# Kernel tuning notes

Measured on AMD Instinct MI355X. Metric: run time of the kernel, lower is better.

The kernel has to match this reference:

```python
import jax, jax.numpy as jnp
import numpy as np

VOCAB = 100000
E = 300          # embedding_size
S = 128          # seq_len
B = 8192         # batch
H1 = 2048
H2 = 2048
C = 1221         # num_classes
PAD = 1          # padding token id (sentence trimmed after last non-1 token)


def setup_inputs() -> dict:
    key = jax.random.key(0)
    ks = jax.random.split(key, 8)
    x = jax.random.randint(ks[0], (S, B), 0, VOCAB, dtype=jnp.int64 if jax.config.jax_enable_x64 else jnp.int32)
    emb = jax.random.normal(ks[1], (VOCAB, E), dtype=jnp.float32) * 0.1
    W1 = jax.random.normal(ks[2], (H1, 2 * E), dtype=jnp.float32) * (1.0 / np.sqrt(2 * E))
    b1 = jnp.zeros((H1,), dtype=jnp.float32)
    W2 = jax.random.normal(ks[3], (H2, H1), dtype=jnp.float32) * (1.0 / np.sqrt(H1))
    b2 = jnp.zeros((H2,), dtype=jnp.float32)
    W_out = jax.random.normal(ks[4], (C, H2), dtype=jnp.float32) * (1.0 / np.sqrt(H2))
    b_out = jnp.zeros((C,), dtype=jnp.float32)
    return {"x": x, "emb": emb, "W1": W1, "b1": b1, "W2": W2, "b2": b2,
            "W_out": W_out, "b_out": b_out}


def reference(x, emb, W1, b1, W2, b2, W_out, b_out):
    # x: [S, B] token ids -> transpose to [B, S] as in torch forward
    xb = x.T                                   # [B, S]
    nonpad = xb != PAD                         # [B, S]
    # index of LAST non-padding token per sentence (torch: (sent != 1).nonzero()[-1])
    last = (S - 1) - jnp.argmax(nonpad[:, ::-1], axis=1)      # [B]
    pos = jnp.arange(S)
    # sentence[:last+1] keeps everything up to and including `last`,
    # including any PAD tokens inside that prefix (faithful to the slice).
    mask = (pos[None, :] <= last[:, None]).astype(emb.dtype)  # [B, S]

    ex = emb[xb]                               # [B, S, E] embedding lookup
    mean = jnp.einsum('bse,bs->be', ex, mask) / jnp.sum(mask, axis=1, keepdims=True)
    feat = jnp.concatenate([ex[:, 0, :], mean], axis=1)       # [B, 2E] (FEE + avg)

    h = jax.nn.relu(feat @ W1.T + b1)          # [B, H1]
    h = jax.nn.relu(h @ W2.T + b2)             # [B, H2]
    out = h @ W_out.T + b_out                  # [B, C]
    return out
```

## Files before the change

kernel.cpp:

```cpp
#include <hip/hip_runtime.h>
#include <hip/hip_bf16.h>

#define S 128
#define BATCH 8192
#define E 300
#define KPAD 640
#define H1 2048
#define H2 2048
#define CLS 1221
#define CPAD 1280
#define PADTOK 1
#define VOCAB 100000

typedef __bf16 bf16x8 __attribute__((ext_vector_type(8)));
typedef float f32x16 __attribute__((ext_vector_type(16)));

__device__ __forceinline__ float b2f(ushort u) {
  union { unsigned int i; float f; } v; v.i = ((unsigned int)u) << 16; return v.f;
}
__device__ __forceinline__ ushort f2b(float f) {
  unsigned int i = __float_as_uint(f);
  unsigned int r = (i + 0x7FFFu + ((i >> 16) & 1u)) >> 16;
  return (ushort)r;
}
__device__ __forceinline__ void async16(const void* g, void* l) {
  __builtin_amdgcn_global_load_lds(
      (__attribute__((address_space(1))) void*)(void*)(const_cast<void*>(g)),
      (__attribute__((address_space(3))) void*)l, 16, 0, 0);
}

#define NQ_EMB (VOCAB * E / 4)
#define NQ_W1  (H1 * KPAD / 4)
#define NQ_W2  (H1 * H2 / 4)
#define NQ_WO  (CPAD * H2 / 4)
#define NQ_XT  (S * BATCH / 4)
#define NQ_TOT (NQ_EMB + NQ_W1 + NQ_W2 + NQ_WO + NQ_XT)

__global__ __launch_bounds__(256) void cvt_all(const float* __restrict__ Ein,
                                               ushort* __restrict__ Eb,
                                               const float* __restrict__ W1,
                                               ushort* __restrict__ W1p,
                                               const float* __restrict__ W2,
                                               ushort* __restrict__ W2b,
                                               const float* __restrict__ Wout,
                                               ushort* __restrict__ Woutp,
                                               const int* __restrict__ x,
                                               int* __restrict__ xT) {
  int q = blockIdx.x * 256 + threadIdx.x;
  if (q < NQ_EMB) {
    float4 v = ((const float4*)Ein)[q];
    ushort4 o;
    o.x = f2b(v.x); o.y = f2b(v.y); o.z = f2b(v.z); o.w = f2b(v.w);
    ((ushort4*)Eb)[q] = o;
    return;
  }
  q -= NQ_EMB;
  if (q < NQ_W1) {
    int row = q / 160;
    int k0 = (q - row * 160) * 4;
    ushort4 o; o.x = 0; o.y = 0; o.z = 0; o.w = 0;
    if (k0 < 2 * E) {
      float4 v = *(const float4*)(W1 + (size_t)row * (2 * E) + k0);
      o.x = f2b(v.x); o.y = f2b(v.y); o.z = f2b(v.z); o.w = f2b(v.w);
    }
    ((ushort4*)W1p)[q] = o;
    return;
  }
  q -= NQ_W1;
  if (q < NQ_W2) {
    float4 v = ((const float4*)W2)[q];
    ushort4 o;
    o.x = f2b(v.x); o.y = f2b(v.y); o.z = f2b(v.z); o.w = f2b(v.w);
    ((ushort4*)W2b)[q] = o;
    return;
  }
  q -= NQ_W2;
  if (q < NQ_WO) {
    int n = (q * 4) >> 11;
    ushort4 o; o.x = 0; o.y = 0; o.z = 0; o.w = 0;
    if (n < CLS) {
      float4 v = ((const float4*)Wout)[q];
      o.x = f2b(v.x); o.y = f2b(v.y); o.z = f2b(v.z); o.w = f2b(v.w);
    }
    ((ushort4*)Woutp)[q] = o;
    return;
  }
  q -= NQ_WO;
  if (q < NQ_XT) {
    int b = q >> 5;
    int t4 = (q & 31) * 4;
    int4 o;
    o.x = x[(size_t)(t4 + 0) * BATCH + b];
    o.y = x[(size_t)(t4 + 1) * BATCH + b];
    o.z = x[(size_t)(t4 + 2) * BATCH + b];
    o.w = x[(size_t)(t4 + 3) * BATCH + b];
    ((int4*)xT)[q] = o;
  }
}

__global__ __launch_bounds__(128) void embed_kernel(const int* __restrict__ xT,
                                                    const ushort* __restrict__ emb,
                                                    ushort* __restrict__ feat) {
  __shared__ uint offs[S];
  __shared__ unsigned long long masks[2];
  const int b = blockIdx.x;
  const int t = threadIdx.x;

  int tok = xT[b * S + t];
  offs[t] = (uint)tok * 600u;
  unsigned long long m = __ballot(tok != PADTOK);
  if ((t & 63) == 0) masks[t >> 6] = m;
  __syncthreads();

  unsigned long long m0 = masks[0], m1 = masks[1];
  int last;
  if (m1)      last = 127 - __clzll(m1);
  else if (m0) last = 63 - __clzll(m0);
  else         last = S - 1;
  const int n = last + 1;
  const float inv = 1.0f / (float)n;

  const int lane = t & 63;
  const int q0 = (t < 64) ? t : (11 + t);
  const bool has2 = (lane < 11);
  const int q1 = q0 + 64;
  const uint off0 = 4u * (uint)q0;
  const uint off1 = 4u * (uint)q1;
  const char* base = (const char*)emb;

  float a0 = 0.f, a1 = 0.f, a2 = 0.f, a3 = 0.f;
  int s = 0;
  for (; s + 16 <= n; s += 16) {
    uint o[16];
#pragma unroll
    for (int j = 0; j < 16; j++) o[j] = offs[s + j];
    ushort2 u[16];
#pragma unroll
    for (int j = 0; j < 16; j++) u[j] = *(const ushort2*)(base + (o[j] + off0));
    ushort2 v[16];
    if (has2) {
#pragma unroll
      for (int j = 0; j < 16; j++) v[j] = *(const ushort2*)(base + (o[j] + off1));
    }
#pragma unroll
    for (int j = 0; j < 16; j++) { a0 += b2f(u[j].x); a1 += b2f(u[j].y); }
    if (has2) {
#pragma unroll
      for (int j = 0; j < 16; j++) { a2 += b2f(v[j].x); a3 += b2f(v[j].y); }
    }
  }
  for (; s < n; s++) {
    uint o = offs[s];
    ushort2 u = *(const ushort2*)(base + (o + off0));
    a0 += b2f(u.x); a1 += b2f(u.y);
    if (has2) {
      ushort2 v0 = *(const ushort2*)(base + (o + off1));
      a2 += b2f(v0.x); a3 += b2f(v0.y);
    }
  }

  ushort* fr = feat + (size_t)b * KPAD;
  ushort2 mo; mo.x = f2b(a0 * inv); mo.y = f2b(a1 * inv);
  *(ushort2*)(fr + E + 2 * q0) = mo;
  if (has2) {
    ushort2 mo2; mo2.x = f2b(a2 * inv); mo2.y = f2b(a3 * inv);
    *(ushort2*)(fr + E + 2 * q1) = mo2;
  }
  const uint o0 = offs[0];
  *(ushort2*)(fr + 2 * q0) = *(const ushort2*)(base + (o0 + off0));
  if (has2) *(ushort2*)(fr + 2 * q1) = *(const ushort2*)(base + (o0 + off1));
  if (t < 20) {
    ushort2 z; z.x = 0; z.y = 0;
    *(ushort2*)(fr + 2 * E + 2 * t) = z;
  }
}

#define BM 128
#define BN 128
#define BK 64

template <bool RELU, bool NGUARD, bool FP32OUT>
__global__ __launch_bounds__(256) void gemm_bt(const ushort* __restrict__ A,
                                               const ushort* __restrict__ B,
                                               const float* __restrict__ bias,
                                               void* __restrict__ Cv,
                                               int K, int lda, int ldb, int ldc,
                                               int Nreal) {
  __shared__ __align__(16) ushort lA[BM * BK];
  __shared__ __align__(16) ushort lB[BN * BK];

  const int tid = threadIdx.x;
  const int wave = tid >> 6;
  const int lane = tid & 63;
  const int m0 = blockIdx.y * BM;
  const int n0 = blockIdx.x * BN;
  const int wm = (wave >> 1) * 64;
  const int wn = (wave & 1) * 64;

  f32x16 acc[2][2];
#pragma unroll
  for (int i = 0; i < 2; i++)
#pragma unroll
    for (int j = 0; j < 2; j++)
#pragma unroll
      for (int r = 0; r < 16; r++) acc[i][j][r] = 0.f;

  const int srow8 = lane >> 3;
  const int kcw = (lane & 7) ^ srow8;

  const int lr = lane & 31;
  const int lk = lane >> 5;
  const int lx = lr & 7;

  for (int k0 = 0; k0 < K; k0 += BK) {
#pragma unroll
    for (int j = 0; j < 4; j++) {
      const int g = wave * 4 + j;
      const int row = g * 8 + srow8;
      async16(A + (size_t)(m0 + row) * lda + k0 + kcw * 8, (void*)&lA[g * 512]);
      async16(B + (size_t)(n0 + row) * ldb + k0 + kcw * 8, (void*)&lB[g * 512]);
    }
    __syncthreads();

#pragma unroll
    for (int ks = 0; ks < 4; ks++) {
      const int kc = ks * 2 + lk;
      bf16x8 af[2], bfr[2];
#pragma unroll
      for (int mi = 0; mi < 2; mi++) {
        const int row = wm + mi * 32 + lr;
        af[mi] = *(const bf16x8*)&lA[(row * 8 + (kc ^ lx)) * 8];
      }
#pragma unroll
      for (int ni = 0; ni < 2; ni++) {
        const int row = wn + ni * 32 + lr;
        bfr[ni] = *(const bf16x8*)&lB[(row * 8 + (kc ^ lx)) * 8];
      }
#pragma unroll
      for (int mi = 0; mi < 2; mi++)
#pragma unroll
        for (int ni = 0; ni < 2; ni++)
          acc[mi][ni] = __builtin_amdgcn_mfma_f32_32x32x16_bf16(
              af[mi], bfr[ni], acc[mi][ni], 0, 0, 0);
    }
    __syncthreads();
  }

#pragma unroll
  for (int ni = 0; ni < 2; ni++) {
    const int col = n0 + wn + ni * 32 + lr;
    const bool ok = (!NGUARD) || (col < Nreal);
    const float bv = ok ? bias[col] : 0.f;
#pragma unroll
    for (int mi = 0; mi < 2; mi++) {
#pragma unroll
      for (int r = 0; r < 16; r++) {
        const int row = m0 + wm + mi * 32 + (r & 3) + 8 * (r >> 2) + 4 * lk;
        float v = acc[mi][ni][r] + bv;
        if (RELU) v = fmaxf(v, 0.f);
        if (ok) {
          if (FP32OUT) ((float*)Cv)[(size_t)row * ldc + col] = v;
          else         ((ushort*)Cv)[(size_t)row * ldc + col] = f2b(v);
        }
      }
    }
  }
}

extern "C" void kernel_launch(void* const* d_in, const int* in_sizes, int n_in,
                              void* d_out, int out_size, void* d_ws, size_t ws_size,
                              hipStream_t stream) {
  const int* x = (const int*)d_in[0];
  const float* emb = (const float*)d_in[1];
  const float* W1 = (const float*)d_in[2];
  const float* b1 = (const float*)d_in[3];
  const float* W2 = (const float*)d_in[4];
  const float* b2 = (const float*)d_in[5];
  const float* Wout = (const float*)d_in[6];
  const float* bout = (const float*)d_in[7];
  float* out = (float*)d_out;

  char* ws = (char*)d_ws;
  ushort* feat = (ushort*)ws;  ws += (size_t)BATCH * KPAD * 2;
  ushort* h1 = (ushort*)ws;    ws += (size_t)BATCH * H1 * 2;
  ushort* h2 = (ushort*)ws;    ws += (size_t)BATCH * H2 * 2;
  ushort* W1p = (ushort*)ws;   ws += (size_t)H1 * KPAD * 2;
  ushort* W2b = (ushort*)ws;   ws += (size_t)H2 * H1 * 2;
  ushort* Woutp = (ushort*)ws; ws += (size_t)CPAD * H2 * 2;
  ushort* Eb = (ushort*)ws;    ws += (size_t)VOCAB * E * 2;
  int* xT = (int*)ws;          ws += (size_t)S * BATCH * 4;

  cvt_all<<<(NQ_TOT + 255) / 256, 256, 0, stream>>>(emb, Eb, W1, W1p, W2, W2b,
                                                    Wout, Woutp, x, xT);
  embed_kernel<<<BATCH, S, 0, stream>>>(xT, Eb, feat);

  gemm_bt<true, false, false><<<dim3(H1 / BN, BATCH / BM), 256, 0, stream>>>(
      feat, W1p, b1, (void*)h1, KPAD, KPAD, KPAD, H1, H1);
  gemm_bt<true, false, false><<<dim3(H2 / BN, BATCH / BM), 256, 0, stream>>>(
      h1, W2b, b2, (void*)h2, H1, H1, H1, H2, H2);
  gemm_bt<false, true, true><<<dim3(CPAD / BN, BATCH / BM), 256, 0, stream>>>(
      h2, Woutp, bout, (void*)out, H2, H2, H2, CLS, CLS);
}
```

Measured before the change: 504.0 us.

## Split embedding sum across two waves by sequence parity with 8-byte loads

The embedding-mean kernel used to split the 300 columns across two waves, each reading 4-byte pairs. Now each wave covers the full row with 8-byte ushort4 loads and handles alternating sequence positions. The two partial sums are combined through shared memory after a barrier. This widens the loads and balances the sequence work, at the cost of one extra sync and an LDS reduction.

```diff
diff --git a/kernel.cpp b/kernel.cpp
--- a/kernel.cpp
+++ b/kernel.cpp
@@ -103,6 +103,7 @@
                                                     ushort* __restrict__ feat) {
   __shared__ uint offs[S];
   __shared__ unsigned long long masks[2];
+  __shared__ __align__(16) float part[76 * 4];
   const int b = blockIdx.x;
   const int t = threadIdx.x;
 
@@ -120,58 +121,84 @@
   const int n = last + 1;
   const float inv = 1.0f / (float)n;
 
+  const int w = t >> 6;
   const int lane = t & 63;
-  const int q0 = (t < 64) ? t : (11 + t);
-  const bool has2 = (lane < 11);
-  const int q1 = q0 + 64;
-  const uint off0 = 4u * (uint)q0;
-  const uint off1 = 4u * (uint)q1;
   const char* base = (const char*)emb;
+  const uint off0 = (uint)lane * 8u;
+  const bool tail = (lane < 11);
+  const uint off1 = 512u + (uint)lane * 8u;
 
   float a0 = 0.f, a1 = 0.f, a2 = 0.f, a3 = 0.f;
-  int s = 0;
-  for (; s + 16 <= n; s += 16) {
-    uint o[16];
-#pragma unroll
-    for (int j = 0; j < 16; j++) o[j] = offs[s + j];
-    ushort2 u[16];
-#pragma unroll
-    for (int j = 0; j < 16; j++) u[j] = *(const ushort2*)(base + (o[j] + off0));
-    ushort2 v[16];
-    if (has2) {
-#pragma unroll
-      for (int j = 0; j < 16; j++) v[j] = *(const ushort2*)(base + (o[j] + off1));
-    }
-#pragma unroll
-    for (int j = 0; j < 16; j++) { a0 += b2f(u[j].x); a1 += b2f(u[j].y); }
-    if (has2) {
-#pragma unroll
-      for (int j = 0; j < 16; j++) { a2 += b2f(v[j].x); a3 += b2f(v[j].y); }
-    }
-  }
-  for (; s < n; s++) {
+  float c0 = 0.f, c1 = 0.f, c2 = 0.f, c3 = 0.f;
+
+  int s = w;
+  for (; s + 14 < n; s += 16) {
+    uint o[8];
+#pragma unroll
+    for (int j = 0; j < 8; j++) o[j] = offs[s + 2 * j];
+    ushort4 u[8];
+#pragma unroll
+    for (int j = 0; j < 8; j++) u[j] = *(const ushort4*)(base + (o[j] + off0));
+    ushort4 v[8];
+    if (tail) {
+#pragma unroll
+      for (int j = 0; j < 8; j++) v[j] = *(const ushort4*)(base + (o[j] + off1));
+    }
+#pragma unroll
+    for (int j = 0; j < 8; j++) {
+      a0 += b2f(u[j].x); a1 += b2f(u[j].y);
+      a2 += b2f(u[j].z); a3 += b2f(u[j].w);
+    }
+    if (tail) {
+#pragma unroll
+      for (int j = 0; j < 8; j++) {
+        c0 += b2f(v[j].x); c1 += b2f(v[j].y);
+        c2 += b2f(v[j].z); c3 += b2f(v[j].w);
+      }
+    }
+  }
+  for (; s < n; s += 2) {
     uint o = offs[s];
-    ushort2 u = *(const ushort2*)(base + (o + off0));
-    a0 += b2f(u.x); a1 += b2f(u.y);
-    if (has2) {
-      ushort2 v0 = *(const ushort2*)(base + (o + off1));
-      a2 += b2f(v0.x); a3 += b2f(v0.y);
-    }
-  }
+    ushort4 u = *(const ushort4*)(base + (o + off0));
+    a0 += b2f(u.x); a1 += b2f(u.y); a2 += b2f(u.z); a3 += b2f(u.w);
+    if (tail) {
+      ushort4 v = *(const ushort4*)(base + (o + off1));
+      c0 += b2f(v.x); c1 += b2f(v.y); c2 += b2f(v.z); c3 += b2f(v.w);
+    }
+  }
+
+  if (w == 1) {
+    float4 av; av.x = a0; av.y = a1; av.z = a2; av.w = a3;
+    *(float4*)&part[lane * 4] = av;
+    if (tail) {
+      float4 cv; cv.x = c0; cv.y = c1; cv.z = c2; cv.w = c3;
+      *(float4*)&part[(64 + lane) * 4] = cv;
+    }
+  }
+  __syncthreads();
 
   ushort* fr = feat + (size_t)b * KPAD;
-  ushort2 mo; mo.x = f2b(a0 * inv); mo.y = f2b(a1 * inv);
-  *(ushort2*)(fr + E + 2 * q0) = mo;
-  if (has2) {
-    ushort2 mo2; mo2.x = f2b(a2 * inv); mo2.y = f2b(a3 * inv);
-    *(ushort2*)(fr + E + 2 * q1) = mo2;
-  }
+  if (w == 0) {
+    float4 pv = *(const float4*)&part[lane * 4];
+    ushort4 mo;
+    mo.x = f2b((a0 + pv.x) * inv); mo.y = f2b((a1 + pv.y) * inv);
+    mo.z = f2b((a2 + pv.z) * inv); mo.w = f2b((a3 + pv.w) * inv);
+    *(ushort4*)(fr + E + lane * 4) = mo;
+    if (tail) {
+      float4 qv = *(const float4*)&part[(64 + lane) * 4];
+      ushort4 mo2;
+      mo2.x = f2b((c0 + qv.x) * inv); mo2.y = f2b((c1 + qv.y) * inv);
+      mo2.z = f2b((c2 + qv.z) * inv); mo2.w = f2b((c3 + qv.w) * inv);
+      *(ushort4*)(fr + E + (64 + lane) * 4) = mo2;
+    }
+  }
+
   const uint o0 = offs[0];
-  *(ushort2*)(fr + 2 * q0) = *(const ushort2*)(base + (o0 + off0));
-  if (has2) *(ushort2*)(fr + 2 * q1) = *(const ushort2*)(base + (o0 + off1));
-  if (t < 20) {
-    ushort2 z; z.x = 0; z.y = 0;
-    *(ushort2*)(fr + 2 * E + 2 * t) = z;
+  if (t < 75) {
+    *(ushort4*)(fr + 4 * t) = *(const ushort4*)(base + (o0 + 8u * (uint)t));
+  } else if (t < 85) {
+    ushort4 z; z.x = 0; z.y = 0; z.z = 0; z.w = 0;
+    *(ushort4*)(fr + 2 * E + 4 * (t - 75)) = z;
   }
 }
 
```

Result: no change. 501.9 us (-0.4%).
